# Kernel optimization log

Hardware: AMD Instinct MI355X
Metric: run time of the kernel (lower is better)

## Reference

```python
import jax, jax.numpy as jnp
import numpy as np

NSIDE = 128
NPIX = 12 * NSIDE * NSIDE          # HEALPix pixel count, nested ordering
WIN = 16                           # window = 4x4 nested child block (w=1)
SHIFT = WIN // 2
EPS = 1e-5


def _ln(x, g, b):
    mu = x.mean(-1, keepdims=True)
    var = ((x - mu) ** 2).mean(-1, keepdims=True)
    return (x - mu) * jax.lax.rsqrt(var + EPS) * g + b


def _window_attn(x, wq, bq, wp, bp, n_heads):
    B, N, C = x.shape
    D = C // n_heads
    nw = N // WIN
    qkv = (x @ wq + bq).reshape(B, nw, WIN, 3, n_heads, D)
    q, k, v = jnp.moveaxis(qkv, 3, 0)
    q = jnp.swapaxes(q, 2, 3)
    k = jnp.swapaxes(k, 2, 3)
    v = jnp.swapaxes(v, 2, 3)
    scores = jnp.einsum('bwhqd,bwhkd->bwhqk', q, k) * (D ** -0.5)
    attn = jax.nn.softmax(scores, axis=-1)
    out = jnp.einsum('bwhqk,bwhkd->bwhqd', attn, v)
    out = jnp.swapaxes(out, 2, 3).reshape(B, N, C)
    return out @ wp + bp


def _transformer_block(x, p, shift, n_heads):
    if shift:
        x = jnp.roll(x, -SHIFT, axis=1)          # cyclic shift along nested index
    x = x + _window_attn(_ln(x, p['ln1_g'], p['ln1_b']),
                         p['w_qkv'], p['b_qkv'], p['w_proj'], p['b_proj'], n_heads)
    h = _ln(x, p['ln2_g'], p['ln2_b'])
    x = x + jax.nn.gelu(h @ p['w_mlp1'] + p['b_mlp1'], approximate=False) @ p['w_mlp2'] + p['b_mlp2']
    if shift:
        x = jnp.roll(x, SHIFT, axis=1)
    return x


def _forward(x, w_ff1, b_ff1, ln1_g, ln1_b, w_qkv, b_qkv, w_proj, b_proj,
             ln2_g, ln2_b, w_mlp1, b_mlp1, w_mlp2, b_mlp2, w_ff2, b_ff2,
             n_heads=4):
    residual = x
    h = jax.nn.gelu(x @ w_ff1 + b_ff1, approximate=False)
    for i, shift in enumerate((False, True)):
        p = dict(ln1_g=ln1_g[i], ln1_b=ln1_b[i], w_qkv=w_qkv[i], b_qkv=b_qkv[i],
                 w_proj=w_proj[i], b_proj=b_proj[i], ln2_g=ln2_g[i], ln2_b=ln2_b[i],
                 w_mlp1=w_mlp1[i], b_mlp1=b_mlp1[i], w_mlp2=w_mlp2[i], b_mlp2=b_mlp2[i])
        h = _transformer_block(h, p, shift, n_heads)
    return residual + h @ w_ff2 + b_ff2


def setup_inputs() -> dict:
    key = jax.random.key(0)
    ks = jax.random.split(key, 8)
    F, C, M = 64, 128, 512  # node_feat_dim, node_hidden_dim, mlp hidden
    s = 0.02
    return {
        'x': jax.random.normal(ks[0], (1, NPIX, F), jnp.float32),
        'w_ff1': jax.random.normal(ks[1], (F, C), jnp.float32) * s,
        'b_ff1': jnp.zeros((C,), jnp.float32),
        'ln1_g': jnp.ones((2, C), jnp.float32),
        'ln1_b': jnp.zeros((2, C), jnp.float32),
        'w_qkv': jax.random.normal(ks[2], (2, C, 3 * C), jnp.float32) * s,
        'b_qkv': jnp.zeros((2, 3 * C), jnp.float32),
        'w_proj': jax.random.normal(ks[3], (2, C, C), jnp.float32) * s,
        'b_proj': jnp.zeros((2, C), jnp.float32),
        'ln2_g': jnp.ones((2, C), jnp.float32),
        'ln2_b': jnp.zeros((2, C), jnp.float32),
        'w_mlp1': jax.random.normal(ks[4], (2, C, M), jnp.float32) * s,
        'b_mlp1': jnp.zeros((2, M), jnp.float32),
        'w_mlp2': jax.random.normal(ks[5], (2, M, C), jnp.float32) * s,
        'b_mlp2': jnp.zeros((2, C), jnp.float32),
        'w_ff2': jax.random.normal(ks[6], (C, F), jnp.float32) * s,
        'b_ff2': jnp.zeros((F,), jnp.float32),
    }


def reference(x, w_ff1, b_ff1, ln1_g, ln1_b, w_qkv, b_qkv, w_proj, b_proj,
              ln2_g, ln2_b, w_mlp1, b_mlp1, w_mlp2, b_mlp2, w_ff2, b_ff2):
    return _forward(x, w_ff1, b_ff1, ln1_g, ln1_b, w_qkv, b_qkv, w_proj, b_proj,
                    ln2_g, ln2_b, w_mlp1, b_mlp1, w_mlp2, b_mlp2, w_ff2, b_ff2)
```

## Files before the change

### kernel.cpp

```cpp
#include <hip/hip_runtime.h>
#include <hip/hip_bf16.h>
#include <math.h>

#define NPIX 196608
#define SCALE_Q 0.17677669529663687f

typedef __attribute__((ext_vector_type(4))) float f32x4;
typedef __attribute__((ext_vector_type(8))) short short8;
typedef __attribute__((ext_vector_type(4))) short short4v;
typedef __hip_bfloat16 bf16;

__device__ __forceinline__ float gelu_f(float x) {
    float yy = 1.5957691216057308f * (x + 0.044715f * x * x * x);
    float e = __expf(yy);
    return x - x * __builtin_amdgcn_rcpf(e + 1.0f);
}
__device__ __forceinline__ float gelu_fast(float x) {
    float e = __expf(-1.702f * x);
    return x * __builtin_amdgcn_rcpf(1.0f + e);
}

__device__ __forceinline__ short bfbits(float f) {
    bf16 h = __float2bfloat16(f);
    return *reinterpret_cast<short*>(&h);
}

__device__ __forceinline__ short8 ldsA(const bf16* buf, int row, int el) {
    return *reinterpret_cast<const short8*>(buf + row * 128 + (el ^ ((row & 7) << 3)));
}
__device__ __forceinline__ short8 ldsA64(const bf16* buf, int row, int el) {
    return *reinterpret_cast<const short8*>(buf + row * 64 + (el ^ ((row & 7) << 3)));
}
__device__ __forceinline__ short8 gld8(const bf16* p) {
    return *reinterpret_cast<const short8*>(p);
}

__device__ __forceinline__ void bar_lds() {
    asm volatile("s_waitcnt lgkmcnt(0)" ::: "memory");
    __builtin_amdgcn_s_barrier();
}

__global__ __launch_bounds__(256) void k_convert(
    const float* __restrict__ wff1, const float* __restrict__ wqkv,
    const float* __restrict__ wproj, const float* __restrict__ wmlp1,
    const float* __restrict__ wmlp2, const float* __restrict__ wff2,
    bf16* __restrict__ dst)
{
    int gid = blockIdx.x * 256 + threadIdx.x;
    if (gid < 8192) {
        int n = gid >> 6, k = gid & 63;
        dst[gid] = __float2bfloat16(wff1[k * 128 + n]);
    } else if (gid < 106496) {
        int r = gid - 8192; int l = r / 49152; r -= l * 49152;
        int n = r >> 7, k = r & 127;
        dst[gid] = __float2bfloat16(wqkv[l * 49152 + k * 384 + n]);
    } else if (gid < 139264) {
        int r = gid - 106496; int l = r / 16384; r -= l * 16384;
        int n = r >> 7, k = r & 127;
        dst[gid] = __float2bfloat16(wproj[l * 16384 + k * 128 + n]);
    } else if (gid < 270336) {
        int r = gid - 139264; int l = r >> 16; r &= 65535;
        int n = r >> 7, k = r & 127;
        dst[gid] = __float2bfloat16(wmlp1[l * 65536 + k * 512 + n]);
    } else if (gid < 401408) {
        int r = gid - 270336; int l = r >> 16; r &= 65535;
        int n = r >> 9, k = r & 511;
        dst[gid] = __float2bfloat16(wmlp2[l * 65536 + k * 128 + n]);
    } else if (gid < 409600) {
        int r = gid - 401408;
        int n = r >> 7, k = r & 127;
        dst[gid] = __float2bfloat16(wff2[k * 64 + n]);
    }
}

template <int OFFSET, int MODE>
__global__ __launch_bounds__(256, 3) void k_block(
    const float* __restrict__ x, float* __restrict__ h,
    const bf16* __restrict__ wf1t, const float* __restrict__ bf1,
    const float* __restrict__ g1, const float* __restrict__ be1,
    const bf16* __restrict__ wqt, const float* __restrict__ bq,
    const bf16* __restrict__ wpt, const float* __restrict__ bp,
    const float* __restrict__ g2, const float* __restrict__ be2,
    const bf16* __restrict__ w1t, const float* __restrict__ b1,
    const bf16* __restrict__ w2t, const float* __restrict__ b2,
    const bf16* __restrict__ wf2t, const float* __restrict__ bf2,
    float* __restrict__ out)
{
    __shared__ __align__(16) bf16 bufA[8192];
    __shared__ __align__(16) bf16 bufB[8192];
    __shared__ __align__(16) bf16 bufC[8192];
    const int tid = threadIdx.x, base = blockIdx.x * 64;
    const int wid = tid >> 6, lrow = tid & 15, lgrp = (tid >> 4) & 3;
    const int cb0 = wid * 32;
    const int hc  = wid * 32;

    f32x4 hraw[2][4];

    if (MODE == 0) {
        short8 wf1[2][2];
#pragma unroll
        for (int nt = 0; nt < 2; ++nt)
#pragma unroll
            for (int kk = 0; kk < 2; ++kk)
                wf1[nt][kk] = gld8(wf1t + (size_t)(cb0 + nt * 16 + lrow) * 64 + kk * 32 + lgrp * 8);
        {
            int row = tid >> 2, q = tid & 3;
#pragma unroll
            for (int s = 0; s < 2; ++s) {
                int gg = q + s * 4;
                const float4* src = reinterpret_cast<const float4*>(x + (size_t)(base + row) * 64 + gg * 8);
                float4 v0 = src[0], v1 = src[1];
                short8 w;
                w[0] = bfbits(v0.x); w[1] = bfbits(v0.y); w[2] = bfbits(v0.z); w[3] = bfbits(v0.w);
                w[4] = bfbits(v1.x); w[5] = bfbits(v1.y); w[6] = bfbits(v1.z); w[7] = bfbits(v1.w);
                *reinterpret_cast<short8*>(&bufC[row * 64 + ((gg * 8) ^ ((row & 7) << 3))]) = w;
            }
        }
        bar_lds();
        short8 xb1[4][2];
#pragma unroll
        for (int tt = 0; tt < 4; ++tt)
#pragma unroll
            for (int kk = 0; kk < 2; ++kk)
                xb1[tt][kk] = ldsA64(bufC, tt * 16 + lrow, kk * 32 + lgrp * 8);
        bar_lds();
#pragma unroll
        for (int nt = 0; nt < 2; ++nt) {
            float4 bv = *reinterpret_cast<const float4*>(bf1 + cb0 + nt * 16 + lgrp * 4);
#pragma unroll
            for (int tt = 0; tt < 4; ++tt) {
                f32x4 d = {0.f, 0.f, 0.f, 0.f};
#pragma unroll
                for (int kk = 0; kk < 2; ++kk)
                    d = __builtin_amdgcn_mfma_f32_16x16x32_bf16(wf1[nt][kk], xb1[tt][kk], d, 0, 0, 0);
                f32x4 r;
                r[0] = gelu_f(d[0] + bv.x); r[1] = gelu_f(d[1] + bv.y);
                r[2] = gelu_f(d[2] + bv.z); r[3] = gelu_f(d[3] + bv.w);
                hraw[nt][tt] = r;
            }
        }
    } else {
#pragma unroll
        for (int nt = 0; nt < 2; ++nt)
#pragma unroll
            for (int tt = 0; tt < 4; ++tt) {
                int tok = base + OFFSET + tt * 16 + lrow; if (tok >= NPIX) tok -= NPIX;
                float4 hv = *reinterpret_cast<const float4*>(h + (size_t)tok * 128 + cb0 + nt * 16 + lgrp * 4);
                f32x4 r; r[0] = hv.x; r[1] = hv.y; r[2] = hv.z; r[3] = hv.w;
                hraw[nt][tt] = r;
            }
    }

    float2* ws = reinterpret_cast<float2*>(bufC);
#pragma unroll
    for (int tt = 0; tt < 4; ++tt) {
        float s = 0.f, q = 0.f;
#pragma unroll
        for (int nt = 0; nt < 2; ++nt)
#pragma unroll
            for (int i = 0; i < 4; ++i) { float v = hraw[nt][tt][i]; s += v; q += v * v; }
        s += __shfl_xor(s, 16, 64); s += __shfl_xor(s, 32, 64);
        q += __shfl_xor(q, 16, 64); q += __shfl_xor(q, 32, 64);
        if (lgrp == 0) { float2 t2; t2.x = s; t2.y = q; ws[wid * 64 + tt * 16 + lrow] = t2; }
    }
    bar_lds();
    {
        float mu[4], rstd[4];
#pragma unroll
        for (int tt = 0; tt < 4; ++tt) {
            float s = 0.f, q = 0.f;
#pragma unroll
            for (int w = 0; w < 4; ++w) {
                float2 t2 = ws[w * 64 + tt * 16 + lrow];
                s += t2.x; q += t2.y;
            }
            float m = s * (1.f / 128.f);
            mu[tt] = m;
            rstd[tt] = rsqrtf(q * (1.f / 128.f) - m * m + 1e-5f);
        }
        float4 gv[2], bev[2];
#pragma unroll
        for (int nt = 0; nt < 2; ++nt) {
            gv[nt]  = *reinterpret_cast<const float4*>(g1 + cb0 + nt * 16 + lgrp * 4);
            bev[nt] = *reinterpret_cast<const float4*>(be1 + cb0 + nt * 16 + lgrp * 4);
        }
#pragma unroll
        for (int nt = 0; nt < 2; ++nt)
#pragma unroll
            for (int tt = 0; tt < 4; ++tt) {
                short4v pk;
                pk[0] = bfbits((hraw[nt][tt][0] - mu[tt]) * rstd[tt] * gv[nt].x + bev[nt].x);
                pk[1] = bfbits((hraw[nt][tt][1] - mu[tt]) * rstd[tt] * gv[nt].y + bev[nt].y);
                pk[2] = bfbits((hraw[nt][tt][2] - mu[tt]) * rstd[tt] * gv[nt].z + bev[nt].z);
                pk[3] = bfbits((hraw[nt][tt][3] - mu[tt]) * rstd[tt] * gv[nt].w + bev[nt].w);
                int row = tt * 16 + lrow;
                int c = cb0 + nt * 16 + lgrp * 4;
                *reinterpret_cast<short4v*>(&bufA[row * 128 + (c ^ ((row & 7) << 3))]) = pk;
            }
    }
    short8 wfp[2][4];
#pragma unroll
    for (int nt = 0; nt < 2; ++nt)
#pragma unroll
        for (int kk = 0; kk < 4; ++kk)
            wfp[nt][kk] = gld8(wpt + (size_t)(cb0 + nt * 16 + lrow) * 128 + kk * 32 + lgrp * 8);
    bar_lds();

    short8 xb[4][4];
#pragma unroll
    for (int tt = 0; tt < 4; ++tt)
#pragma unroll
        for (int kk = 0; kk < 4; ++kk)
            xb[tt][kk] = ldsA(bufA, tt * 16 + lrow, kk * 32 + lgrp * 8);
    bar_lds();

#pragma unroll
    for (int qt = 0; qt < 2; ++qt) {
        const int cb = hc + qt * 16;
        float4 bqv = *reinterpret_cast<const float4*>(bq + cb + lgrp * 4);
        short8 wf[4];
#pragma unroll
        for (int kk = 0; kk < 4; ++kk)
            wf[kk] = gld8(wqt + (size_t)(cb + lrow) * 128 + kk * 32 + lgrp * 8);
#pragma unroll
        for (int tt = 0; tt < 4; ++tt) {
            f32x4 d = {0.f, 0.f, 0.f, 0.f};
#pragma unroll
            for (int kk = 0; kk < 4; ++kk)
                d = __builtin_amdgcn_mfma_f32_16x16x32_bf16(wf[kk], xb[tt][kk], d, 0, 0, 0);
            int row = tt * 16 + lrow;
            int c = cb + lgrp * 4;
            short4v pk;
            pk[0] = bfbits((d[0] + bqv.x) * SCALE_Q); pk[1] = bfbits((d[1] + bqv.y) * SCALE_Q);
            pk[2] = bfbits((d[2] + bqv.z) * SCALE_Q); pk[3] = bfbits((d[3] + bqv.w) * SCALE_Q);
            *reinterpret_cast<short4v*>(&bufA[row * 128 + (c ^ ((row & 7) << 3))]) = pk;
        }
    }
#pragma unroll
    for (int kt = 0; kt < 2; ++kt) {
        const int cb = hc + kt * 16;
        float4 bqv = *reinterpret_cast<const float4*>(bq + 128 + cb + lgrp * 4);
        short8 wf[4];
#pragma unroll
        for (int kk = 0; kk < 4; ++kk)
            wf[kk] = gld8(wqt + (size_t)(128 + cb + lrow) * 128 + kk * 32 + lgrp * 8);
#pragma unroll
        for (int tt = 0; tt < 4; ++tt) {
            f32x4 d = {0.f, 0.f, 0.f, 0.f};
#pragma unroll
            for (int kk = 0; kk < 4; ++kk)
                d = __builtin_amdgcn_mfma_f32_16x16x32_bf16(wf[kk], xb[tt][kk], d, 0, 0, 0);
            int row = tt * 16 + lrow;
            int c = cb + lgrp * 4;
            short4v pk;
            pk[0] = bfbits(d[0] + bqv.x); pk[1] = bfbits(d[1] + bqv.y);
            pk[2] = bfbits(d[2] + bqv.z); pk[3] = bfbits(d[3] + bqv.w);
            *reinterpret_cast<short4v*>(&bufB[row * 128 + (c ^ ((row & 7) << 3))]) = pk;
        }
    }
    bf16* vt = bufC + wid * 2048;
#pragma unroll
    for (int vt_ = 0; vt_ < 2; ++vt_) {
        const int cb = hc + vt_ * 16;
        float4 bqv = *reinterpret_cast<const float4*>(bq + 256 + cb + lgrp * 4);
        short8 wf[4];
#pragma unroll
        for (int kk = 0; kk < 4; ++kk)
            wf[kk] = gld8(wqt + (size_t)(256 + cb + lrow) * 128 + kk * 32 + lgrp * 8);
#pragma unroll
        for (int tt = 0; tt < 4; ++tt) {
            f32x4 d = {0.f, 0.f, 0.f, 0.f};
#pragma unroll
            for (int kk = 0; kk < 4; ++kk)
                d = __builtin_amdgcn_mfma_f32_16x16x32_bf16(wf[kk], xb[tt][kk], d, 0, 0, 0);
#pragma unroll
            for (int i = 0; i < 4; ++i)
                vt[(vt_ * 16 + lgrp * 4 + i) * 64 + tt * 16 + lrow] =
                    __float2bfloat16(d[i] + ((const float*)&bqv)[i]);
        }
    }

#pragma unroll
    for (int tt = 0; tt < 4; ++tt) {
        const int row = tt * 16 + lrow;
        const int swr = (lrow & 7) << 3;
        short8 aq = *reinterpret_cast<const short8*>(&bufA[row * 128 + ((hc + lgrp * 8) ^ swr)]);
        short8 bk = *reinterpret_cast<const short8*>(&bufB[row * 128 + ((hc + lgrp * 8) ^ swr)]);
        f32x4 z = {0.f, 0.f, 0.f, 0.f};
        f32x4 s = __builtin_amdgcn_mfma_f32_16x16x32_bf16(bk, aq, z, 0, 0, 0);
        float m_ = fmaxf(fmaxf(s[0], s[1]), fmaxf(s[2], s[3]));
        m_ = fmaxf(m_, __shfl_xor(m_, 16, 64));
        m_ = fmaxf(m_, __shfl_xor(m_, 32, 64));
        float e0 = __expf(s[0] - m_), e1 = __expf(s[1] - m_);
        float e2 = __expf(s[2] - m_), e3 = __expf(s[3] - m_);
        float sum = e0 + e1 + e2 + e3;
        sum += __shfl_xor(sum, 16, 64);
        sum += __shfl_xor(sum, 32, 64);
        float r = __builtin_amdgcn_rcpf(sum);
        short4v pp;
        pp[0] = bfbits(e0 * r); pp[1] = bfbits(e1 * r);
        pp[2] = bfbits(e2 * r); pp[3] = bfbits(e3 * r);
        *reinterpret_cast<short4v*>(&bufA[row * 128 + ((hc + lgrp * 4) ^ swr)]) = pp;

        short8 z8 = {0, 0, 0, 0, 0, 0, 0, 0};
        short8 bp_ = z8;
        if (lgrp < 2)
            bp_ = *reinterpret_cast<const short8*>(&bufA[row * 128 + ((hc + lgrp * 8) ^ swr)]);
#pragma unroll
        for (int dt = 0; dt < 2; ++dt) {
            short8 av = z8;
            if (lgrp < 2)
                av = *reinterpret_cast<const short8*>(&vt[(dt * 16 + lrow) * 64 + tt * 16 + lgrp * 8]);
            f32x4 o = __builtin_amdgcn_mfma_f32_16x16x32_bf16(av, bp_, z, 0, 0, 0);
            short4v pk;
            pk[0] = bfbits(o[0]); pk[1] = bfbits(o[1]); pk[2] = bfbits(o[2]); pk[3] = bfbits(o[3]);
            *reinterpret_cast<short4v*>(&bufA[row * 128 + ((hc + dt * 16 + lgrp * 4) ^ swr)]) = pk;
        }
    }
    bar_lds();

    short8 af[4][4];
#pragma unroll
    for (int tt = 0; tt < 4; ++tt)
#pragma unroll
        for (int kk = 0; kk < 4; ++kk)
            af[tt][kk] = ldsA(bufA, tt * 16 + lrow, kk * 32 + lgrp * 8);
    f32x4 hres[2][4];
#pragma unroll
    for (int nt = 0; nt < 2; ++nt) {
        float4 bpv = *reinterpret_cast<const float4*>(bp + cb0 + nt * 16 + lgrp * 4);
#pragma unroll
        for (int tt = 0; tt < 4; ++tt) {
            f32x4 d = {0.f, 0.f, 0.f, 0.f};
#pragma unroll
            for (int kk = 0; kk < 4; ++kk)
                d = __builtin_amdgcn_mfma_f32_16x16x32_bf16(wfp[nt][kk], af[tt][kk], d, 0, 0, 0);
            f32x4 r = hraw[nt][tt];
            r[0] += bpv.x + d[0]; r[1] += bpv.y + d[1];
            r[2] += bpv.z + d[2]; r[3] += bpv.w + d[3];
            hres[nt][tt] = r;
        }
    }

#pragma unroll
    for (int tt = 0; tt < 4; ++tt) {
        float s = 0.f, q = 0.f;
#pragma unroll
        for (int nt = 0; nt < 2; ++nt)
#pragma unroll
            for (int i = 0; i < 4; ++i) { float v = hres[nt][tt][i]; s += v; q += v * v; }
        s += __shfl_xor(s, 16, 64); s += __shfl_xor(s, 32, 64);
        q += __shfl_xor(q, 16, 64); q += __shfl_xor(q, 32, 64);
        if (lgrp == 0) { float2 t2; t2.x = s; t2.y = q; ws[wid * 64 + tt * 16 + lrow] = t2; }
    }
    bar_lds();
    short8 w1f[2][2][4];
    {
        float mu[4], rstd[4];
#pragma unroll
        for (int tt = 0; tt < 4; ++tt) {
            float s = 0.f, q = 0.f;
#pragma unroll
            for (int w = 0; w < 4; ++w) {
                float2 t2 = ws[w * 64 + tt * 16 + lrow];
                s += t2.x; q += t2.y;
            }
            float m = s * (1.f / 128.f);
            mu[tt] = m;
            rstd[tt] = rsqrtf(q * (1.f / 128.f) - m * m + 1e-5f);
        }
        float4 gv[2], bev[2];
#pragma unroll
        for (int nt = 0; nt < 2; ++nt) {
            gv[nt]  = *reinterpret_cast<const float4*>(g2 + cb0 + nt * 16 + lgrp * 4);
            bev[nt] = *reinterpret_cast<const float4*>(be2 + cb0 + nt * 16 + lgrp * 4);
        }
#pragma unroll
        for (int nt = 0; nt < 2; ++nt)
#pragma unroll
            for (int tt = 0; tt < 4; ++tt) {
                short4v pk;
                pk[0] = bfbits((hres[nt][tt][0] - mu[tt]) * rstd[tt] * gv[nt].x + bev[nt].x);
                pk[1] = bfbits((hres[nt][tt][1] - mu[tt]) * rstd[tt] * gv[nt].y + bev[nt].y);
                pk[2] = bfbits((hres[nt][tt][2] - mu[tt]) * rstd[tt] * gv[nt].z + bev[nt].z);
                pk[3] = bfbits((hres[nt][tt][3] - mu[tt]) * rstd[tt] * gv[nt].w + bev[nt].w);
                int row = tt * 16 + lrow;
                int c = cb0 + nt * 16 + lgrp * 4;
                *reinterpret_cast<short4v*>(&bufB[row * 128 + (c ^ ((row & 7) << 3))]) = pk;
            }
    }
#pragma unroll
    for (int nt = 0; nt < 2; ++nt)
#pragma unroll
        for (int kk = 0; kk < 4; ++kk)
            w1f[0][nt][kk] = gld8(w1t + (size_t)(cb0 + nt * 16 + lrow) * 128 + kk * 32 + lgrp * 8);
    bar_lds();

    f32x4 acc2[2][4];
#pragma unroll
    for (int nt = 0; nt < 2; ++nt)
#pragma unroll
        for (int tt = 0; tt < 4; ++tt) acc2[nt][tt] = (f32x4){0.f, 0.f, 0.f, 0.f};

#pragma unroll
    for (int ch = 0; ch < 4; ++ch) {
        bf16* UB = (ch & 1) ? bufC : bufA;
        short8 w2f[2][4];
#pragma unroll
        for (int nt = 0; nt < 2; ++nt)
#pragma unroll
            for (int kk = 0; kk < 4; ++kk)
                w2f[nt][kk] = gld8(w2t + (size_t)(cb0 + nt * 16 + lrow) * 512 + ch * 128 + kk * 32 + lgrp * 8);
        float4 b1v[2];
#pragma unroll
        for (int nt = 0; nt < 2; ++nt)
            b1v[nt] = *reinterpret_cast<const float4*>(b1 + ch * 128 + cb0 + nt * 16 + lgrp * 4);
#pragma unroll
        for (int tt = 0; tt < 4; ++tt) {
            short8 xf[4];
#pragma unroll
            for (int kk = 0; kk < 4; ++kk)
                xf[kk] = ldsA(bufB, tt * 16 + lrow, kk * 32 + lgrp * 8);
#pragma unroll
            for (int nt = 0; nt < 2; ++nt) {
                f32x4 d = {0.f, 0.f, 0.f, 0.f};
#pragma unroll
                for (int kk = 0; kk < 4; ++kk)
                    d = __builtin_amdgcn_mfma_f32_16x16x32_bf16(w1f[ch & 1][nt][kk], xf[kk], d, 0, 0, 0);
                short4v pk;
                pk[0] = bfbits(gelu_fast(d[0] + b1v[nt].x)); pk[1] = bfbits(gelu_fast(d[1] + b1v[nt].y));
                pk[2] = bfbits(gelu_fast(d[2] + b1v[nt].z)); pk[3] = bfbits(gelu_fast(d[3] + b1v[nt].w));
                int row = tt * 16 + lrow;
                int c = cb0 + nt * 16 + lgrp * 4;
                *reinterpret_cast<short4v*>(&UB[row * 128 + (c ^ ((row & 7) << 3))]) = pk;
            }
        }
        if (ch < 3) {
#pragma unroll
            for (int nt = 0; nt < 2; ++nt)
#pragma unroll
                for (int kk = 0; kk < 4; ++kk)
                    w1f[(ch + 1) & 1][nt][kk] =
                        gld8(w1t + (size_t)((ch + 1) * 128 + cb0 + nt * 16 + lrow) * 128 + kk * 32 + lgrp * 8);
        }
        bar_lds();
#pragma unroll
        for (int tt = 0; tt < 4; ++tt) {
            short8 uf[4];
#pragma unroll
            for (int kk = 0; kk < 4; ++kk)
                uf[kk] = ldsA(UB, tt * 16 + lrow, kk * 32 + lgrp * 8);
#pragma unroll
            for (int nt = 0; nt < 2; ++nt)
#pragma unroll
                for (int kk = 0; kk < 4; ++kk)
                    acc2[nt][tt] = __builtin_amdgcn_mfma_f32_16x16x32_bf16(
                        w2f[nt][kk], uf[kk], acc2[nt][tt], 0, 0, 0);
        }
    }

    if (MODE == 0) {
#pragma unroll
        for (int nt = 0; nt < 2; ++nt) {
            const int n0 = cb0 + nt * 16 + lgrp * 4;
            float4 b2v = *reinterpret_cast<const float4*>(b2 + n0);
#pragma unroll
            for (int tt = 0; tt < 4; ++tt) {
                int tok = base + OFFSET + tt * 16 + lrow; if (tok >= NPIX) tok -= NPIX;
                float4 ov;
                ov.x = hres[nt][tt][0] + b2v.x + acc2[nt][tt][0];
                ov.y = hres[nt][tt][1] + b2v.y + acc2[nt][tt][1];
                ov.z = hres[nt][tt][2] + b2v.z + acc2[nt][tt][2];
                ov.w = hres[nt][tt][3] + b2v.w + acc2[nt][tt][3];
                *reinterpret_cast<float4*>(h + (size_t)tok * 128 + n0) = ov;
            }
        }
    } else {
        short8 wff[4];
#pragma unroll
        for (int kk = 0; kk < 4; ++kk)
            wff[kk] = gld8(wf2t + (size_t)(wid * 16 + lrow) * 128 + kk * 32 + lgrp * 8);
        float4 xv[4];
#pragma unroll
        for (int tt = 0; tt < 4; ++tt) {
            int tok = base + OFFSET + tt * 16 + lrow; if (tok >= NPIX) tok -= NPIX;
            xv[tt] = *reinterpret_cast<const float4*>(x + (size_t)tok * 64 + wid * 16 + lgrp * 4);
        }
        bar_lds();
#pragma unroll
        for (int nt = 0; nt < 2; ++nt) {
            const int n0 = cb0 + nt * 16 + lgrp * 4;
            float4 b2v = *reinterpret_cast<const float4*>(b2 + n0);
#pragma unroll
            for (int tt = 0; tt < 4; ++tt) {
                short4v pk;
                pk[0] = bfbits(hres[nt][tt][0] + b2v.x + acc2[nt][tt][0]);
                pk[1] = bfbits(hres[nt][tt][1] + b2v.y + acc2[nt][tt][1]);
                pk[2] = bfbits(hres[nt][tt][2] + b2v.z + acc2[nt][tt][2]);
                pk[3] = bfbits(hres[nt][tt][3] + b2v.w + acc2[nt][tt][3]);
                int row = tt * 16 + lrow;
                int c = cb0 + nt * 16 + lgrp * 4;
                *reinterpret_cast<short4v*>(&bufB[row * 128 + (c ^ ((row & 7) << 3))]) = pk;
            }
        }
        bar_lds();
        float4 bfv = *reinterpret_cast<const float4*>(bf2 + wid * 16 + lgrp * 4);
#pragma unroll
        for (int tt = 0; tt < 4; ++tt) {
            short8 bfr[4];
#pragma unroll
            for (int kk = 0; kk < 4; ++kk)
                bfr[kk] = ldsA(bufB, tt * 16 + lrow, kk * 32 + lgrp * 8);
            f32x4 d = {0.f, 0.f, 0.f, 0.f};
#pragma unroll
            for (int kk = 0; kk < 4; ++kk)
                d = __builtin_amdgcn_mfma_f32_16x16x32_bf16(wff[kk], bfr[kk], d, 0, 0, 0);
            int tok = base + OFFSET + tt * 16 + lrow; if (tok >= NPIX) tok -= NPIX;
            float4 ov;
            ov.x = xv[tt].x + bfv.x + d[0]; ov.y = xv[tt].y + bfv.y + d[1];
            ov.z = xv[tt].z + bfv.z + d[2]; ov.w = xv[tt].w + bfv.w + d[3];
            *reinterpret_cast<float4*>(out + (size_t)tok * 64 + wid * 16 + lgrp * 4) = ov;
        }
    }
}

extern "C" void kernel_launch(void* const* d_in, const int* in_sizes, int n_in,
                              void* d_out, int out_size, void* d_ws, size_t ws_size,
                              hipStream_t stream) {
    (void)in_sizes; (void)n_in; (void)out_size; (void)ws_size;
    const float* x      = (const float*)d_in[0];
    const float* w_ff1  = (const float*)d_in[1];
    const float* b_ff1  = (const float*)d_in[2];
    const float* ln1_g  = (const float*)d_in[3];
    const float* ln1_b  = (const float*)d_in[4];
    const float* w_qkv  = (const float*)d_in[5];
    const float* b_qkv  = (const float*)d_in[6];
    const float* w_proj = (const float*)d_in[7];
    const float* b_proj = (const float*)d_in[8];
    const float* ln2_g  = (const float*)d_in[9];
    const float* ln2_b  = (const float*)d_in[10];
    const float* w_mlp1 = (const float*)d_in[11];
    const float* b_mlp1 = (const float*)d_in[12];
    const float* w_mlp2 = (const float*)d_in[13];
    const float* b_mlp2 = (const float*)d_in[14];
    const float* w_ff2  = (const float*)d_in[15];
    const float* b_ff2  = (const float*)d_in[16];
    float* out = (float*)d_out;

    float* h = (float*)d_ws;
    bf16* wbf = (bf16*)((char*)d_ws + (size_t)NPIX * 128 * 4);
    bf16* ff1t  = wbf;
    bf16* qkvt  = wbf + 8192;
    bf16* projt = wbf + 106496;
    bf16* mlp1t = wbf + 139264;
    bf16* mlp2t = wbf + 270336;
    bf16* ff2t  = wbf + 401408;

    k_convert<<<1600, dim3(256), 0, stream>>>(w_ff1, w_qkv, w_proj, w_mlp1, w_mlp2, w_ff2, wbf);

    const int NB = NPIX / 64;
    k_block<0, 0><<<NB, dim3(256), 0, stream>>>(x, h,
        ff1t, b_ff1,
        ln1_g, ln1_b, qkvt, b_qkv, projt, b_proj,
        ln2_g, ln2_b, mlp1t, b_mlp1, mlp2t, b_mlp2,
        ff2t, b_ff2, out);

    k_block<8, 1><<<NB, dim3(256), 0, stream>>>(x, h,
        ff1t, b_ff1,
        ln1_g + 128, ln1_b + 128, qkvt + 49152, b_qkv + 384, projt + 16384, b_proj + 128,
        ln2_g + 128, ln2_b + 128, mlp1t + 65536, b_mlp1 + 512, mlp2t + 65536, b_mlp2 + 128,
        ff2t, b_ff2, out);
}
```

Baseline: 407.7 us.

## Shrink LDS footprint by halving V-transpose buffer and single-buffering MLP hidden tile

Cuts the third shared buffer from 16KB to 8KB by processing the V transpose in two half-tiles of 32 tokens, with an XOR swizzle on the per-wave V storage. The MLP hidden chunk now always goes to bufA instead of ping-ponging with bufC, so an extra barrier is added per chunk. LayerNorm partial sums move to bufB and bufC, and some barriers are removed. Lower LDS per block is meant to let more blocks fit per CU, at the cost of extra synchronization in the MLP loop and more serialized attention work.

```diff
diff --git a/kernel.cpp b/kernel.cpp
--- a/kernel.cpp
+++ b/kernel.cpp
@@ -88,7 +88,7 @@
 {
     __shared__ __align__(16) bf16 bufA[8192];
     __shared__ __align__(16) bf16 bufB[8192];
-    __shared__ __align__(16) bf16 bufC[8192];
+    __shared__ __align__(16) bf16 bufC[4096];
     const int tid = threadIdx.x, base = blockIdx.x * 64;
     const int wid = tid >> 6, lrow = tid & 15, lgrp = (tid >> 4) & 3;
     const int cb0 = wid * 32;
@@ -123,7 +123,6 @@
 #pragma unroll
             for (int kk = 0; kk < 2; ++kk)
                 xb1[tt][kk] = ldsA64(bufC, tt * 16 + lrow, kk * 32 + lgrp * 8);
-        bar_lds();
 #pragma unroll
         for (int nt = 0; nt < 2; ++nt) {
             float4 bv = *reinterpret_cast<const float4*>(bf1 + cb0 + nt * 16 + lgrp * 4);
@@ -151,7 +150,7 @@
             }
     }
 
-    float2* ws = reinterpret_cast<float2*>(bufC);
+    float2* ws1 = reinterpret_cast<float2*>(bufB);
 #pragma unroll
     for (int tt = 0; tt < 4; ++tt) {
         float s = 0.f, q = 0.f;
@@ -161,7 +160,7 @@
             for (int i = 0; i < 4; ++i) { float v = hraw[nt][tt][i]; s += v; q += v * v; }
         s += __shfl_xor(s, 16, 64); s += __shfl_xor(s, 32, 64);
         q += __shfl_xor(q, 16, 64); q += __shfl_xor(q, 32, 64);
-        if (lgrp == 0) { float2 t2; t2.x = s; t2.y = q; ws[wid * 64 + tt * 16 + lrow] = t2; }
+        if (lgrp == 0) { float2 t2; t2.x = s; t2.y = q; ws1[wid * 64 + tt * 16 + lrow] = t2; }
     }
     bar_lds();
     {
@@ -171,7 +170,7 @@
             float s = 0.f, q = 0.f;
 #pragma unroll
             for (int w = 0; w < 4; ++w) {
-                float2 t2 = ws[w * 64 + tt * 16 + lrow];
+                float2 t2 = ws1[w * 64 + tt * 16 + lrow];
                 s += t2.x; q += t2.y;
             }
             float m = s * (1.f / 128.f);
@@ -258,63 +257,70 @@
             *reinterpret_cast<short4v*>(&bufB[row * 128 + (c ^ ((row & 7) << 3))]) = pk;
         }
     }
-    bf16* vt = bufC + wid * 2048;
-#pragma unroll
-    for (int vt_ = 0; vt_ < 2; ++vt_) {
-        const int cb = hc + vt_ * 16;
-        float4 bqv = *reinterpret_cast<const float4*>(bq + 256 + cb + lgrp * 4);
-        short8 wf[4];
-#pragma unroll
-        for (int kk = 0; kk < 4; ++kk)
-            wf[kk] = gld8(wqt + (size_t)(256 + cb + lrow) * 128 + kk * 32 + lgrp * 8);
-#pragma unroll
-        for (int tt = 0; tt < 4; ++tt) {
-            f32x4 d = {0.f, 0.f, 0.f, 0.f};
-#pragma unroll
-            for (int kk = 0; kk < 4; ++kk)
-                d = __builtin_amdgcn_mfma_f32_16x16x32_bf16(wf[kk], xb[tt][kk], d, 0, 0, 0);
-#pragma unroll
-            for (int i = 0; i < 4; ++i)
-                vt[(vt_ * 16 + lgrp * 4 + i) * 64 + tt * 16 + lrow] =
-                    __float2bfloat16(d[i] + ((const float*)&bqv)[i]);
-        }
-    }
-
-#pragma unroll
-    for (int tt = 0; tt < 4; ++tt) {
-        const int row = tt * 16 + lrow;
-        const int swr = (lrow & 7) << 3;
-        short8 aq = *reinterpret_cast<const short8*>(&bufA[row * 128 + ((hc + lgrp * 8) ^ swr)]);
-        short8 bk = *reinterpret_cast<const short8*>(&bufB[row * 128 + ((hc + lgrp * 8) ^ swr)]);
-        f32x4 z = {0.f, 0.f, 0.f, 0.f};
-        f32x4 s = __builtin_amdgcn_mfma_f32_16x16x32_bf16(bk, aq, z, 0, 0, 0);
-        float m_ = fmaxf(fmaxf(s[0], s[1]), fmaxf(s[2], s[3]));
-        m_ = fmaxf(m_, __shfl_xor(m_, 16, 64));
-        m_ = fmaxf(m_, __shfl_xor(m_, 32, 64));
-        float e0 = __expf(s[0] - m_), e1 = __expf(s[1] - m_);
-        float e2 = __expf(s[2] - m_), e3 = __expf(s[3] - m_);
-        float sum = e0 + e1 + e2 + e3;
-        sum += __shfl_xor(sum, 16, 64);
-        sum += __shfl_xor(sum, 32, 64);
-        float r = __builtin_amdgcn_rcpf(sum);
-        short4v pp;
-        pp[0] = bfbits(e0 * r); pp[1] = bfbits(e1 * r);
-        pp[2] = bfbits(e2 * r); pp[3] = bfbits(e3 * r);
-        *reinterpret_cast<short4v*>(&bufA[row * 128 + ((hc + lgrp * 4) ^ swr)]) = pp;
-
-        short8 z8 = {0, 0, 0, 0, 0, 0, 0, 0};
-        short8 bp_ = z8;
-        if (lgrp < 2)
-            bp_ = *reinterpret_cast<const short8*>(&bufA[row * 128 + ((hc + lgrp * 8) ^ swr)]);
-#pragma unroll
-        for (int dt = 0; dt < 2; ++dt) {
-            short8 av = z8;
+    bf16* vt = bufC + wid * 1024;
+#pragma unroll
+    for (int half = 0; half < 2; ++half) {
+#pragma unroll
+        for (int vt_ = 0; vt_ < 2; ++vt_) {
+            const int cb = hc + vt_ * 16;
+            float4 bqv = *reinterpret_cast<const float4*>(bq + 256 + cb + lgrp * 4);
+            short8 wf[4];
+#pragma unroll
+            for (int kk = 0; kk < 4; ++kk)
+                wf[kk] = gld8(wqt + (size_t)(256 + cb + lrow) * 128 + kk * 32 + lgrp * 8);
+#pragma unroll
+            for (int t2 = 0; t2 < 2; ++t2) {
+                const int tt = half * 2 + t2;
+                f32x4 d = {0.f, 0.f, 0.f, 0.f};
+#pragma unroll
+                for (int kk = 0; kk < 4; ++kk)
+                    d = __builtin_amdgcn_mfma_f32_16x16x32_bf16(wf[kk], xb[tt][kk], d, 0, 0, 0);
+#pragma unroll
+                for (int i = 0; i < 4; ++i) {
+                    int dd = vt_ * 16 + lgrp * 4 + i;
+                    vt[dd * 32 + ((t2 * 16 + lrow) ^ ((dd & 3) << 3))] =
+                        __float2bfloat16(d[i] + ((const float*)&bqv)[i]);
+                }
+            }
+        }
+#pragma unroll
+        for (int t2 = 0; t2 < 2; ++t2) {
+            const int tt = half * 2 + t2;
+            const int row = tt * 16 + lrow;
+            const int swr = (lrow & 7) << 3;
+            short8 aq = *reinterpret_cast<const short8*>(&bufA[row * 128 + ((hc + lgrp * 8) ^ swr)]);
+            short8 bk = *reinterpret_cast<const short8*>(&bufB[row * 128 + ((hc + lgrp * 8) ^ swr)]);
+            f32x4 z = {0.f, 0.f, 0.f, 0.f};
+            f32x4 s = __builtin_amdgcn_mfma_f32_16x16x32_bf16(bk, aq, z, 0, 0, 0);
+            float m_ = fmaxf(fmaxf(s[0], s[1]), fmaxf(s[2], s[3]));
+            m_ = fmaxf(m_, __shfl_xor(m_, 16, 64));
+            m_ = fmaxf(m_, __shfl_xor(m_, 32, 64));
+            float e0 = __expf(s[0] - m_), e1 = __expf(s[1] - m_);
+            float e2 = __expf(s[2] - m_), e3 = __expf(s[3] - m_);
+            float sum = e0 + e1 + e2 + e3;
+            sum += __shfl_xor(sum, 16, 64);
+            sum += __shfl_xor(sum, 32, 64);
+            float r = __builtin_amdgcn_rcpf(sum);
+            short4v pp;
+            pp[0] = bfbits(e0 * r); pp[1] = bfbits(e1 * r);
+            pp[2] = bfbits(e2 * r); pp[3] = bfbits(e3 * r);
+            *reinterpret_cast<short4v*>(&bufA[row * 128 + ((hc + lgrp * 4) ^ swr)]) = pp;
+
+            short8 z8 = {0, 0, 0, 0, 0, 0, 0, 0};
+            short8 bp_ = z8;
             if (lgrp < 2)
-                av = *reinterpret_cast<const short8*>(&vt[(dt * 16 + lrow) * 64 + tt * 16 + lgrp * 8]);
-            f32x4 o = __builtin_amdgcn_mfma_f32_16x16x32_bf16(av, bp_, z, 0, 0, 0);
-            short4v pk;
-            pk[0] = bfbits(o[0]); pk[1] = bfbits(o[1]); pk[2] = bfbits(o[2]); pk[3] = bfbits(o[3]);
-            *reinterpret_cast<short4v*>(&bufA[row * 128 + ((hc + dt * 16 + lgrp * 4) ^ swr)]) = pk;
+                bp_ = *reinterpret_cast<const short8*>(&bufA[row * 128 + ((hc + lgrp * 8) ^ swr)]);
+#pragma unroll
+            for (int dt = 0; dt < 2; ++dt) {
+                short8 av = z8;
+                if (lgrp < 2)
+                    av = *reinterpret_cast<const short8*>(
+                        &vt[(dt * 16 + lrow) * 32 + ((t2 * 16 + lgrp * 8) ^ ((lrow & 3) << 3))]);
+                f32x4 o = __builtin_amdgcn_mfma_f32_16x16x32_bf16(av, bp_, z, 0, 0, 0);
+                short4v pk;
+                pk[0] = bfbits(o[0]); pk[1] = bfbits(o[1]); pk[2] = bfbits(o[2]); pk[3] = bfbits(o[3]);
+                *reinterpret_cast<short4v*>(&bufA[row * 128 + ((hc + dt * 16 + lgrp * 4) ^ swr)]) = pk;
+            }
         }
     }
     bar_lds();
@@ -342,6 +348,7 @@
         }
     }
 
+    float2* ws2 = reinterpret_cast<float2*>(bufC);
 #pragma unroll
     for (int tt = 0; tt < 4; ++tt) {
         float s = 0.f, q = 0.f;
@@ -351,7 +358,7 @@
             for (int i = 0; i < 4; ++i) { float v = hres[nt][tt][i]; s += v; q += v * v; }
         s += __shfl_xor(s, 16, 64); s += __shfl_xor(s, 32, 64);
         q += __shfl_xor(q, 16, 64); q += __shfl_xor(q, 32, 64);
-        if (lgrp == 0) { float2 t2; t2.x = s; t2.y = q; ws[wid * 64 + tt * 16 + lrow] = t2; }
+        if (lgrp == 0) { float2 t2; t2.x = s; t2.y = q; ws2[wid * 64 + tt * 16 + lrow] = t2; }
     }
     bar_lds();
     short8 w1f[2][2][4];
@@ -362,7 +369,7 @@
             float s = 0.f, q = 0.f;
 #pragma unroll
             for (int w = 0; w < 4; ++w) {
-                float2 t2 = ws[w * 64 + tt * 16 + lrow];
+                float2 t2 = ws2[w * 64 + tt * 16 + lrow];
                 s += t2.x; q += t2.y;
             }
             float m = s * (1.f / 128.f);
@@ -404,7 +411,6 @@
 
 #pragma unroll
     for (int ch = 0; ch < 4; ++ch) {
-        bf16* UB = (ch & 1) ? bufC : bufA;
         short8 w2f[2][4];
 #pragma unroll
         for (int nt = 0; nt < 2; ++nt)
@@ -432,7 +438,7 @@
                 pk[2] = bfbits(gelu_fast(d[2] + b1v[nt].z)); pk[3] = bfbits(gelu_fast(d[3] + b1v[nt].w));
                 int row = tt * 16 + lrow;
                 int c = cb0 + nt * 16 + lgrp * 4;
-                *reinterpret_cast<short4v*>(&UB[row * 128 + (c ^ ((row & 7) << 3))]) = pk;
+                *reinterpret_cast<short4v*>(&bufA[row * 128 + (c ^ ((row & 7) << 3))]) = pk;
             }
         }
         if (ch < 3) {
@@ -449,7 +455,7 @@
             short8 uf[4];
 #pragma unroll
             for (int kk = 0; kk < 4; ++kk)
-                uf[kk] = ldsA(UB, tt * 16 + lrow, kk * 32 + lgrp * 8);
+                uf[kk] = ldsA(bufA, tt * 16 + lrow, kk * 32 + lgrp * 8);
 #pragma unroll
             for (int nt = 0; nt < 2; ++nt)
 #pragma unroll
@@ -457,6 +463,7 @@
                     acc2[nt][tt] = __builtin_amdgcn_mfma_f32_16x16x32_bf16(
                         w2f[nt][kk], uf[kk], acc2[nt][tt], 0, 0, 0);
         }
+        if (ch < 3) bar_lds();
     }
 
     if (MODE == 0) {
@@ -486,7 +493,6 @@
             int tok = base + OFFSET + tt * 16 + lrow; if (tok >= NPIX) tok -= NPIX;
             xv[tt] = *reinterpret_cast<const float4*>(x + (size_t)tok * 64 + wid * 16 + lgrp * 4);
         }
-        bar_lds();
 #pragma unroll
         for (int nt = 0; nt < 2; ++nt) {
             const int n0 = cb0 + nt * 16 + lgrp * 4;
```

New measurement: 412.6 us. Within noise of the previous version (+1.2%).
